# Optimization experiments

Measured on AMD Instinct MI355X. Metric: run time of the kernel, lower is better.

The kernel has to match this reference:

```python
import jax, jax.numpy as jnp
import numpy as np

SAMP_RATE = 44100.0
HARMONIC_NUM = 8
SINE_AMP = 0.1
NOISE_STD = 0.003
VOICED_THRESHOLD = 0.0


def setup_inputs() -> dict:
    key = jax.random.key(0)
    k_f0, k_mask, k_ri, k_noise = jax.random.split(key, 4)
    B, T, UPP = 16, 1000, 256
    H = HARMONIC_NUM + 1
    f0 = jax.random.uniform(k_f0, (B, T), dtype=jnp.float32) * 400.0
    voiced = jax.random.uniform(k_mask, (B, T)) > 0.2
    f0 = jnp.where(voiced, f0, 0.0)
    # random initial phases; harmonic 0 has zero offset (rand_ini[:, 0] = 0)
    rand_ini = jax.random.uniform(k_ri, (B, H), dtype=jnp.float32)
    rand_ini = rand_ini.at[:, 0].set(0.0)
    noise = jax.random.normal(k_noise, (B, T * UPP, H), dtype=jnp.float32)
    return {"f0": f0, "rand_ini": rand_ini, "noise": noise, "upp": UPP}


def reference(f0, rand_ini, noise, upp):
    # nearest-neighbor upsample along time: each frame repeated `upp` times
    f0_up = jnp.repeat(f0, upp, axis=1)                      # (B, T_up)
    uv = (f0_up > VOICED_THRESHOLD).astype(f0.dtype)[..., None]  # (B, T_up, 1)
    harmonics = jnp.arange(1, HARMONIC_NUM + 2, dtype=f0.dtype)  # (H,)
    f0_harm = f0_up[..., None] * harmonics                   # (B, T_up, H)
    phase = jnp.cumsum(f0_harm / SAMP_RATE, axis=1)          # (B, T_up, H)
    phase = phase + rand_ini[:, None, :]
    sine_waves = jnp.sin(2.0 * jnp.pi * phase) * SINE_AMP
    noise_amp = uv * NOISE_STD + (1.0 - uv) * (SINE_AMP / 3.0)
    return sine_waves * uv + noise_amp * noise
```

## Files before the change

### kernel.cpp

```cpp
#include <hip/hip_runtime.h>


constexpr int B     = 16;
constexpr int T     = 1000;
constexpr int UPP   = 256;
constexpr int H     = 9;
constexpr int FPB   = 8;
constexpr int FRAME = UPP * H;
constexpr int NF4   = FPB * FRAME / 4;
constexpr int THR   = 512;
constexpr int K     = NF4 / THR;

typedef float f32x4 __attribute__((ext_vector_type(4)));

__global__ __launch_bounds__(1024)
void sinegen_scan_kernel(const float* __restrict__ f0,
                         double* __restrict__ S ) {
    const int b = blockIdx.x;
    const int t = threadIdx.x;
    __shared__ double lds[1024];

    double d = 0.0;
    if (t < T) d = 256.0 * (double)f0[b * T + t];
    lds[t] = d;
    __syncthreads();

    for (int off = 1; off < 1024; off <<= 1) {
        double add = (t >= off) ? lds[t - off] : 0.0;
        __syncthreads();
        lds[t] += add;
        __syncthreads();
    }
    if (t < T) S[b * T + t] = (t > 0) ? lds[t - 1] : 0.0;
}

__global__ __launch_bounds__(THR, 6)
void sinegen_emit_kernel(const float* __restrict__ f0,
                         const float* __restrict__ rand_ini,
                         const float* __restrict__ noise,
                         const double* __restrict__ S,
                         float* __restrict__ out) {
    const int blk = blockIdx.x;
    const int tid = threadIdx.x;

    __shared__ f32x4 MD[FPB * H];

    if (tid < FPB * H) {
        const int q  = tid / H;
        const int h  = tid - q * H;
        const int fg = blk * FPB + q;
        const int b  = fg / T;
        const float  f0v = f0[fg];
        const double kh  = (double)(h + 1) * (1.0 / 44100.0);
        const double md  = S[fg] * kh + (double)rand_ini[b * H + h];
        const double dd  = (double)f0v * kh;
        const bool   v   = (f0v > 0.0f);
        f32x4 w;
        w.x = (float)(dd - floor(dd));
        w.y = (float)(md - floor(md));
        w.z = v ? 0.1f   : 0.0f;
        w.w = v ? 0.003f : (float)(0.1 / 3.0);
        MD[tid] = w;
    }
    __syncthreads();

    const float* nbase = noise + (size_t)blk * (FPB * FRAME);
    float*       obase = out   + (size_t)blk * (FPB * FRAME);

    f32x4 nz[K];
    #pragma unroll
    for (int k = 0; k < K; ++k)
        nz[k] = *(const f32x4*)(nbase + (k * THR + tid) * 4);

    #pragma unroll
    for (int k = 0; k < K; ++k) {
        const int idx = k * THR + tid;
        const int q   = idx / (FRAME / 4);
        const int r   = idx - q * (FRAME / 4);
        f32x4 o;
        #pragma unroll
        for (int j = 0; j < 4; ++j) {
            const int   e  = r * 4 + j;
            const int   u  = e / 9;
            const int   h  = e - u * 9;
            const f32x4 md = MD[q * H + h];
            const float p  = fmaf((float)(u + 1), md.x, md.y);
            const float fr = __builtin_amdgcn_fractf(p);
            float s;
            asm("v_sin_f32 %0, %1" : "=v"(s) : "v"(fr));
            o[j] = fmaf(md.w, nz[k][j], md.z * s);
        }
        __builtin_nontemporal_store(o, (f32x4*)(obase + idx * 4));
    }
}

extern "C" void kernel_launch(void* const* d_in, const int* in_sizes, int n_in,
                              void* d_out, int out_size, void* d_ws, size_t ws_size,
                              hipStream_t stream) {
    const float* f0       = (const float*)d_in[0];
    const float* rand_ini = (const float*)d_in[1];
    const float* noise    = (const float*)d_in[2];
    float*       out      = (float*)d_out;
    double*      Sws      = (double*)d_ws;

    sinegen_scan_kernel<<<B, 1024, 0, stream>>>(f0, Sws);
    sinegen_emit_kernel<<<(B * T) / FPB, THR, 0, stream>>>(f0, rand_ini, noise,
                                                           Sws, out);
}
```

Before: 53.45 us.

## Fuse prefix-scan into emit kernel via per-block redundant reductions

Removes the separate scan kernel and its double-precision workspace. Each emit block now computes the prefix sum of f0 up to its first frame with a block-wide reduction, then adds the frames within the block serially. This removes one kernel launch and the dependency between the two kernels, at the cost of redundant reads of f0 rows (up to 1000 floats per block) and extra syncs before the streaming work begins.

```diff
diff --git a/kernel.cpp b/kernel.cpp
--- a/kernel.cpp
+++ b/kernel.cpp
@@ -6,6 +6,7 @@
 constexpr int UPP   = 256;
 constexpr int H     = 9;
 constexpr int FPB   = 8;
+constexpr int BPR   = T / FPB;
 constexpr int FRAME = UPP * H;
 constexpr int NF4   = FPB * FRAME / 4;
 constexpr int THR   = 512;
@@ -13,46 +14,46 @@
 
 typedef float f32x4 __attribute__((ext_vector_type(4)));
 
-__global__ __launch_bounds__(1024)
-void sinegen_scan_kernel(const float* __restrict__ f0,
-                         double* __restrict__ S ) {
-    const int b = blockIdx.x;
-    const int t = threadIdx.x;
-    __shared__ double lds[1024];
-
-    double d = 0.0;
-    if (t < T) d = 256.0 * (double)f0[b * T + t];
-    lds[t] = d;
-    __syncthreads();
-
-    for (int off = 1; off < 1024; off <<= 1) {
-        double add = (t >= off) ? lds[t - off] : 0.0;
-        __syncthreads();
-        lds[t] += add;
-        __syncthreads();
-    }
-    if (t < T) S[b * T + t] = (t > 0) ? lds[t - 1] : 0.0;
-}
-
 __global__ __launch_bounds__(THR, 6)
-void sinegen_emit_kernel(const float* __restrict__ f0,
-                         const float* __restrict__ rand_ini,
-                         const float* __restrict__ noise,
-                         const double* __restrict__ S,
-                         float* __restrict__ out) {
+void sinegen_fused_kernel(const float* __restrict__ f0,
+                          const float* __restrict__ rand_ini,
+                          const float* __restrict__ noise,
+                          float* __restrict__ out) {
     const int blk = blockIdx.x;
     const int tid = threadIdx.x;
+    const int b   = blk / BPR;
+    const int t0  = (blk - b * BPR) * FPB;
 
-    __shared__ f32x4 MD[FPB * H];
+    __shared__ double wsum[THR / 64];
+    __shared__ double f0d[FPB];
+    __shared__ double Sblk;
+    __shared__ f32x4  MD[FPB * H];
+
+    const float* f0row = f0 + b * T;
+
+    double part = 0.0;
+    for (int t = tid; t < t0; t += THR) part += (double)f0row[t];
+    #pragma unroll
+    for (int off = 32; off > 0; off >>= 1) part += __shfl_down(part, off, 64);
+    if ((tid & 63) == 0) wsum[tid >> 6] = part;
+    if (tid < FPB) f0d[tid] = 256.0 * (double)f0row[t0 + tid];
+    __syncthreads();
+    if (tid == 0) {
+        double s = 0.0;
+        #pragma unroll
+        for (int w = 0; w < THR / 64; ++w) s += wsum[w];
+        Sblk = 256.0 * s;
+    }
+    __syncthreads();
 
     if (tid < FPB * H) {
         const int q  = tid / H;
         const int h  = tid - q * H;
-        const int fg = blk * FPB + q;
-        const int b  = fg / T;
-        const float  f0v = f0[fg];
+        double Sq = Sblk;
+        for (int i = 0; i < q; ++i) Sq += f0d[i];
+        const float  f0v = f0row[t0 + q];
         const double kh  = (double)(h + 1) * (1.0 / 44100.0);
-        const double md  = S[fg] * kh + (double)rand_ini[b * H + h];
+        const double md  = Sq * kh + (double)rand_ini[b * H + h];
         const double dd  = (double)f0v * kh;
         const bool   v   = (f0v > 0.0f);
         f32x4 w;
@@ -101,9 +102,7 @@
     const float* rand_ini = (const float*)d_in[1];
     const float* noise    = (const float*)d_in[2];
     float*       out      = (float*)d_out;
-    double*      Sws      = (double*)d_ws;
 
-    sinegen_scan_kernel<<<B, 1024, 0, stream>>>(f0, Sws);
-    sinegen_emit_kernel<<<(B * T) / FPB, THR, 0, stream>>>(f0, rand_ini, noise,
-                                                           Sws, out);
+    sinegen_fused_kernel<<<(B * T) / FPB, THR, 0, stream>>>(f0, rand_ini,
+                                                            noise, out);
 }
```

Result: faster. 49.76 us (-6.9%).
